# Kernel optimization log

Hardware: AMD Instinct MI355X
Metric: run time of the kernel (lower is better)

Reference implementation:

```python
import jax, jax.numpy as jnp
import numpy as np

NUM_FEATURES = 4
LATENT = 16
HIDDEN = 128
N_PIECES = 20
B, P = 8192, 128


def setup_inputs() -> dict:
    key = jax.random.key(0)
    ks = jax.random.split(key, 8)
    s = lambda fan_in: 1.0 / np.sqrt(fan_in)
    return {
        "x": jax.random.normal(ks[0], (B, P * NUM_FEATURES), jnp.float32),
        "W1": jax.random.normal(ks[1], (NUM_FEATURES, HIDDEN), jnp.float32) * s(NUM_FEATURES),
        "b1": jnp.zeros((HIDDEN,), jnp.float32),
        "W2": jax.random.normal(ks[2], (HIDDEN, HIDDEN), jnp.float32) * s(HIDDEN),
        "b2": jnp.zeros((HIDDEN,), jnp.float32),
        "W3": jax.random.normal(ks[3], (HIDDEN, 2 * LATENT), jnp.float32) * s(HIDDEN),
        "b3": jnp.zeros((2 * LATENT,), jnp.float32),
        "pool_weight": jax.random.normal(ks[4], (2 * LATENT, N_PIECES + 1), jnp.float32) * 0.1,
        "eps": jax.random.normal(ks[5], (B, LATENT), jnp.float32),
    }


def _fspool_weights(pool_weight, set_size):
    # piecewise-linear interpolation of pool_weight over normalized rank positions
    pos = jnp.arange(set_size, dtype=jnp.float32) / (set_size - 1) * N_PIECES  # [P]
    idx = jnp.clip(pos.astype(jnp.int32), 0, N_PIECES)
    frac = pos - idx.astype(jnp.float32)
    left = pool_weight[:, idx]                                   # [C, P]
    right = pool_weight[:, jnp.clip(idx + 1, 0, N_PIECES)]       # [C, P]
    return (1.0 - frac) * left + frac * right                    # [C, P]


def reference(x, W1, b1, W2, b2, W3, b3, pool_weight, eps):
    # per-particle shared MLP, batched over particles (B, P, F) -> (B, P, 2L)
    h = x.reshape(B, P, NUM_FEATURES)
    h = jax.nn.relu(jnp.einsum("bpf,fh->bph", h, W1) + b1)
    h = jax.nn.relu(jnp.einsum("bph,hk->bpk", h, W2) + b2)
    h = jnp.einsum("bph,hc->bpc", h, W3) + b3                    # [B, P, 2L]
    z = jnp.transpose(h, (0, 2, 1))                              # [B, 2L, P]
    # FSPool: descending featurewise sort + rank-weighted sum over set dim
    z_sorted = jnp.flip(jnp.sort(z, axis=-1), axis=-1)           # [B, 2L, P]
    w = _fspool_weights(pool_weight, P)                          # [2L, P]
    pooled = jnp.sum(z_sorted * w[None], axis=-1)                # [B, 2L]
    mus = pooled[:, ::2]
    logvars = pooled[:, 1::2]
    samples = mus + eps * jnp.exp(0.5 * logvars)
    return (mus, logvars, samples)
```

## Files before the change

kernel.cpp:

```cpp
#include <hip/hip_runtime.h>

#define B_TOT 8192
#define NB    16
#define NPCS  20

typedef __attribute__((ext_vector_type(8))) __fp16 f16x8;
typedef __attribute__((ext_vector_type(4))) float f32x4;
typedef __attribute__((ext_vector_type(2))) __fp16 fp16x2;

__device__ __forceinline__ unsigned pkmax(unsigned a, unsigned b) {
    unsigned d; asm("v_pk_max_f16 %0, %1, %2" : "=v"(d) : "v"(a), "v"(b)); return d;
}
__device__ __forceinline__ unsigned pkmin(unsigned a, unsigned b) {
    unsigned d; asm("v_pk_min_f16 %0, %1, %2" : "=v"(d) : "v"(a), "v"(b)); return d;
}
__device__ __forceinline__ unsigned pkrne(float a, float b) {
    fp16x2 h;
    h.x = (__fp16)a;
    h.y = (__fp16)b;
    return __builtin_bit_cast(unsigned, h);
}
__device__ __forceinline__ unsigned pkrtz(float a, float b) {
    return __builtin_bit_cast(unsigned, __builtin_amdgcn_cvt_pkrtz(a, b));
}
__device__ __forceinline__ float asf(unsigned u) { return __builtin_bit_cast(float, u); }
__device__ __forceinline__ unsigned asu(float f) { return __builtin_bit_cast(unsigned, f); }
__device__ __forceinline__ fp16x2 ash2(unsigned u) { return __builtin_bit_cast(fp16x2, u); }
__device__ __forceinline__ unsigned asu2(fp16x2 h) { return __builtin_bit_cast(unsigned, h); }

template<int CTRL>
__device__ __forceinline__ unsigned dppmov(unsigned v) {
    return (unsigned)__builtin_amdgcn_mov_dpp((int)v, CTRL, 0xf, 0xf, true);
}
__device__ __forceinline__ unsigned xlane(unsigned v, int lm) {
    switch (lm) {
    case 1:  return dppmov<0xB1>(v);
    case 2:  return dppmov<0x4E>(v);
    case 4:  return (unsigned)__builtin_amdgcn_ds_swizzle((int)v, 0x101F);
    default: return dppmov<0x128>(v);
    }
}
__device__ __forceinline__ float xlanef(float v, int lm) { return asf(xlane(asu(v), lm)); }

#define WS_W3T 32768
#define WS_WSP 40960
#define WS_W1A 57344
#define WS_B1F 61440

__device__ __forceinline__ unsigned packh2(float lo, float hi) {
    unsigned short a = __builtin_bit_cast(unsigned short, (__fp16)lo);
    unsigned short b = __builtin_bit_cast(unsigned short, (__fp16)hi);
    return (unsigned)a | ((unsigned)b << 16);
}

__device__ __forceinline__ int piperm(int j) {
    return (j & 0x60) | ((j & 0x0C) << 1) | ((j & 0x10) >> 2) | (j & 3);
}

__global__ void prep_kernel(const float* __restrict__ W1, const float* __restrict__ b1,
                            const float* __restrict__ W2, const float* __restrict__ W3,
                            const float* __restrict__ pw, void* __restrict__ ws)
{
    const int t = blockIdx.x * 256 + threadIdx.x;
    __fp16* w2t = (__fp16*)ws;
    __fp16* w3t = (__fp16*)((char*)ws + WS_W3T);
    float* wsp  = (float*)((char*)ws + WS_WSP);
    unsigned* w1a = (unsigned*)((char*)ws + WS_W1A);
    unsigned* b1f = (unsigned*)((char*)ws + WS_B1F);
    if (t < 16384) {
        int j = t >> 7, k = t & 127;
        w2t[t] = (__fp16)W2[k * 128 + piperm(j)];
    } else if (t < 20480) {
        int o = t - 16384, c = o >> 7, k = o & 127;
        w3t[o] = (__fp16)W3[k * 32 + c];
    } else if (t < 24576) {
        int o = t - 20480, c = o >> 7, p = o & 127;
        float pos = (float)p * (20.0f / 127.0f);
        int ip = min((int)pos, NPCS);
        float fr = pos - (float)ip;
        int ipb = min(ip + 1, NPCS);
        wsp[o] = (1.0f - fr) * pw[c * 21 + ip] + fr * pw[c * 21 + ipb];
    } else if (t < 25600) {
        int idx = t - 24576;
        int ht = idx >> 7, lane = (idx >> 1) & 63, pair = idx & 1;
        int quad = lane >> 4, l16 = lane & 15;
        unsigned val = 0;
        if (quad == 0) {
            int sh = piperm(16 * ht + l16);
            val = packh2(W1[(2 * pair) * 128 + sh], W1[(2 * pair + 1) * 128 + sh]);
        }
        w1a[idx] = val;
    } else if (t < 26112) {
        int idx = t - 25600;
        int ht = idx >> 6, lane = idx & 63;
        int quad = lane >> 4, l16 = lane & 15;
        unsigned val = 0;
        if (quad == 0) {
            int sh = piperm(16 * ht + l16);
            val = packh2(b1[sh], 0.0f);
        }
        b1f[idx] = val;
    }
}

#define L_SZP0 32768
#define L_SZP1 41216
#define L_POOL 49664

__global__ __launch_bounds__(256, 2) void enc_kernel(
    const float* __restrict__ x,   const float* __restrict__ b1g,
    const float* __restrict__ b2g, const float* __restrict__ b3g,
    const float* __restrict__ eps, const void* __restrict__ ws,
    float* __restrict__ out)
{
    __shared__ __align__(16) char smem[51712];

    const int tid  = threadIdx.x;
    const int wv   = tid >> 6;
    const int lane = tid & 63;
    const int l16  = lane & 15;
    const int quad = lane >> 4;
    const int b0   = blockIdx.x * NB;

    {
        const uint4* src = (const uint4*)ws;
#pragma unroll
        for (int it = 0; it < 8; ++it) {
            int idx = tid + it * 256;
            int j = idx >> 4, ch = idx & 15;
            *(uint4*)(smem + j * 256 + ((ch ^ (j & 15)) * 16)) = src[idx];
        }
    }

    f16x8 w3f[2][4];
    {
        const __fp16* w3t = (const __fp16*)((const char*)ws + WS_W3T);
#pragma unroll
        for (int mt2 = 0; mt2 < 2; ++mt2)
#pragma unroll
            for (int kt = 0; kt < 4; ++kt)
                w3f[mt2][kt] = *(const f16x8*)(w3t + (mt2 * 16 + l16) * 128 + kt * 32 + quad * 8);
    }
    union WF { unsigned u[4]; f16x8 v; } w1f[8];
    {
        const unsigned* w1a = (const unsigned*)((const char*)ws + WS_W1A);
        const unsigned* b1f = (const unsigned*)((const char*)ws + WS_B1F);
#pragma unroll
        for (int ht = 0; ht < 8; ++ht) {
            uint2 w01 = *(const uint2*)(w1a + ht * 128 + lane * 2);
            w1f[ht].u[0] = w01.x;
            w1f[ht].u[1] = w01.y;
            w1f[ht].u[2] = b1f[ht * 64 + lane];
            w1f[ht].u[3] = 0;
        }
    }
    f32x4 b3acc[2];
    {
        float4 t0 = *(const float4*)(b3g + quad * 4);
        float4 t1 = *(const float4*)(b3g + 16 + quad * 4);
        b3acc[0] = (f32x4){t0.x, t0.y, t0.z, t0.w};
        b3acc[1] = (f32x4){t1.x, t1.y, t1.z, t1.w};
    }
    f32x4 b2acc[8];
#pragma unroll
    for (int nt = 0; nt < 8; ++nt) {
        float4 t4 = *(const float4*)(b2g + (nt >> 1) * 32 + quad * 8 + (nt & 1) * 4);
        b2acc[nt] = (f32x4){t4.x, t4.y, t4.z, t4.w};
    }

    const int pr = wv * 4 + quad;
    float wE[8], wO[8];
    {
        const float* wsp = (const float*)((const char*)ws + WS_WSP);
        float4 e0 = *(const float4*)(wsp + (2 * pr) * 128 + l16 * 8);
        float4 e1 = *(const float4*)(wsp + (2 * pr) * 128 + l16 * 8 + 4);
        float4 o0 = *(const float4*)(wsp + (2 * pr + 1) * 128 + l16 * 8);
        float4 o1 = *(const float4*)(wsp + (2 * pr + 1) * 128 + l16 * 8 + 4);
        wE[0]=e0.x; wE[1]=e0.y; wE[2]=e0.z; wE[3]=e0.w; wE[4]=e1.x; wE[5]=e1.y; wE[6]=e1.z; wE[7]=e1.w;
        wO[0]=o0.x; wO[1]=o0.y; wO[2]=o0.z; wO[3]=o0.w; wO[4]=o1.x; wO[5]=o1.y; wO[6]=o1.z; wO[7]=o1.w;
    }

    const int ib = l16 * 8;
    const unsigned sfl8  = (ib & 8)  ? 0x80008000u : 0u;
    const unsigned sfl16 = (ib & 16) ? 0x80008000u : 0u;
    const unsigned sfl32 = (ib & 32) ? 0x80008000u : 0u;
    const unsigned sfl64 = (ib & 64) ? 0x80008000u : 0u;

    __syncthreads();

    unsigned* szpA  = (unsigned*)(smem + L_SZP0);
    unsigned* szpB  = (unsigned*)(smem + L_SZP1);
    float*    spool = (float*)(smem + L_POOL);

    union XB { unsigned u[4]; f16x8 v; } xb0, xb1;
    xb0.u[2] = 0x3C003C00u; xb0.u[3] = 0;
    xb1.u[2] = 0x3C003C00u; xb1.u[3] = 0;
    const f32x4 zc = (f32x4){0.f, 0.f, 0.f, 0.f};

    const float* xptr = x + (size_t)b0 * 512 + (wv * 32 + l16) * 4;
    float4 xv0 = *(const float4*)(xptr);
    float4 xv1 = *(const float4*)(xptr + 64);

    auto do_gemms = [&](unsigned* __restrict__ szpW, int pfIdx) {
        xb0.u[0] = pkrtz(xv0.x, xv0.y);
        xb0.u[1] = pkrtz(xv0.z, xv0.w);
        xb1.u[0] = pkrtz(xv1.x, xv1.y);
        xb1.u[1] = pkrtz(xv1.z, xv1.w);

        const int pfc = pfIdx < NB - 1 ? pfIdx : NB - 1;
        xv0 = *(const float4*)(xptr + pfc * 512);
        xv1 = *(const float4*)(xptr + pfc * 512 + 64);

        union AF { unsigned u[4]; f16x8 v; } a1[2][4];
#pragma unroll
        for (int ht = 0; ht < 8; ++ht) {
            f32x4 d0 = __builtin_amdgcn_mfma_f32_16x16x32_f16(w1f[ht].v, xb0.v, zc, 0, 0, 0);
            f32x4 d1 = __builtin_amdgcn_mfma_f32_16x16x32_f16(w1f[ht].v, xb1.v, zc, 0, 0, 0);
            const int kt = ht >> 1, jb = 2 * (ht & 1);
            a1[0][kt].u[jb]     = pkmax(pkrtz(d0[0], d0[1]), 0u);
            a1[0][kt].u[jb + 1] = pkmax(pkrtz(d0[2], d0[3]), 0u);
            a1[1][kt].u[jb]     = pkmax(pkrtz(d1[0], d1[1]), 0u);
            a1[1][kt].u[jb + 1] = pkmax(pkrtz(d1[2], d1[3]), 0u);
        }

        f32x4 acc2[2][8];
#pragma unroll
        for (int kt = 0; kt < 4; ++kt)
#pragma unroll
            for (int nt = 0; nt < 8; ++nt) {
                const int j = nt * 16 + l16;
                const int phys = (kt * 4 + quad) ^ l16;
                f16x8 wf = *(const f16x8*)(smem + j * 256 + phys * 16);
                if (kt == 0) {
                    acc2[0][nt] = __builtin_amdgcn_mfma_f32_16x16x32_f16(wf, a1[0][0].v, b2acc[nt], 0, 0, 0);
                    acc2[1][nt] = __builtin_amdgcn_mfma_f32_16x16x32_f16(wf, a1[1][0].v, b2acc[nt], 0, 0, 0);
                } else {
                    acc2[0][nt] = __builtin_amdgcn_mfma_f32_16x16x32_f16(wf, a1[0][kt].v, acc2[0][nt], 0, 0, 0);
                    acc2[1][nt] = __builtin_amdgcn_mfma_f32_16x16x32_f16(wf, a1[1][kt].v, acc2[1][nt], 0, 0, 0);
                }
            }

#pragma unroll
        for (int mt = 0; mt < 2; ++mt) {
            unsigned pkx[8], pky[8];
#pragma unroll
            for (int nt = 0; nt < 8; ++nt) {
                pkx[nt] = pkmax(pkrtz(acc2[mt][nt][0], acc2[mt][nt][1]), 0u);
                pky[nt] = pkmax(pkrtz(acc2[mt][nt][2], acc2[mt][nt][3]), 0u);
            }
            union A3 { unsigned u[4]; f16x8 v; } a3[4];
#pragma unroll
            for (int kt = 0; kt < 4; ++kt) {
                a3[kt].u[0] = pkx[2 * kt];
                a3[kt].u[1] = pky[2 * kt];
                a3[kt].u[2] = pkx[2 * kt + 1];
                a3[kt].u[3] = pky[2 * kt + 1];
            }
            const int colbase = wv * 32 + mt * 16;
#pragma unroll
            for (int mt2 = 0; mt2 < 2; ++mt2) {
                f32x4 acc = __builtin_amdgcn_mfma_f32_16x16x32_f16(w3f[mt2][0], a3[0].v, b3acc[mt2], 0, 0, 0);
#pragma unroll
                for (int kt = 1; kt < 4; ++kt)
                    acc = __builtin_amdgcn_mfma_f32_16x16x32_f16(w3f[mt2][kt], a3[kt].v, acc, 0, 0, 0);
                const int prw = 8 * mt2 + 2 * quad;
                szpW[prw * 132 + colbase + l16]       = pkrne(acc[0], acc[1]);
                szpW[(prw + 1) * 132 + colbase + l16] = pkrne(acc[2], acc[3]);
            }
        }
    };

    auto do_sort = [&](const unsigned* __restrict__ szpR, int e) {
        unsigned v[8];
        {
            const unsigned* zp = szpR + pr * 132 + l16 * 8;
            uint4 za = *(const uint4*)zp;
            uint4 zb = *(const uint4*)(zp + 4);
            v[0]=za.x; v[1]=za.y; v[2]=za.z; v[3]=za.w;
            v[4]=zb.x; v[5]=zb.y; v[6]=zb.z; v[7]=zb.w;
        }
#pragma unroll
        for (int k = 2; k <= 128; k <<= 1) {
#pragma unroll
            for (int j = 64; j >= 1; j >>= 1) {
                if (j >= k) continue;
                if (j >= 8) {
                    const bool km = ((ib & k) == 0) != ((ib & j) != 0);
                    const int lm = j >> 3;
#pragma unroll
                    for (int r = 0; r < 8; ++r) {
                        unsigned p = xlane(v[r], lm);
                        unsigned mx = pkmax(v[r], p), mn = pkmin(v[r], p);
                        v[r] = km ? mx : mn;
                    }
                } else if (k <= 4) {
#pragma unroll
                    for (int a = 0; a < 8; ++a) {
                        if (a & j) continue;
                        const int bx = a | j;
                        unsigned mx = pkmax(v[a], v[bx]), mn = pkmin(v[a], v[bx]);
                        if ((a & k) == 0) { v[a] = mx; v[bx] = mn; }
                        else              { v[a] = mn; v[bx] = mx; }
                    }
                } else {
                    const unsigned sfl = (k == 8) ? sfl8 : (k == 16) ? sfl16 :
                                         (k == 32) ? sfl32 : (k == 64) ? sfl64 : 0u;
                    if (j == 4 && k != 128) {
#pragma unroll
                        for (int r = 0; r < 8; ++r) v[r] ^= sfl;
                    }
#pragma unroll
                    for (int a = 0; a < 8; ++a) {
                        if (a & j) continue;
                        const int bx = a | j;
                        unsigned mx = pkmax(v[a], v[bx]), mn = pkmin(v[a], v[bx]);
                        v[a] = mx; v[bx] = mn;
                    }
                    if (j == 1 && k != 128) {
#pragma unroll
                        for (int r = 0; r < 8; ++r) v[r] ^= sfl;
                    }
                }
            }
        }

        float sE = 0.f, sO = 0.f;
#pragma unroll
        for (int r = 0; r < 8; ++r) {
            const fp16x2 hv = ash2(v[r]);
            sE = fmaf(wE[r], (float)hv.x, sE);
            sO = fmaf(wO[r], (float)hv.y, sO);
        }
#pragma unroll
        for (int d = 8; d >= 1; d >>= 1) {
            sE += xlanef(sE, d);
            sO += xlanef(sO, d);
        }
        if (l16 == 0) {
            spool[e * 32 + 2 * pr]     = sE;
            spool[e * 32 + 2 * pr + 1] = sO;
        }
    };

    do_gemms(szpA, 1);
    __syncthreads();

    for (int e = 0; e < NB - 1; ++e) {
        unsigned* srd = (e & 1) ? szpB : szpA;
        unsigned* dwr = (e & 1) ? szpA : szpB;
        do_gemms(dwr, e + 2);
        do_sort(srd, e);
        __syncthreads();
    }
    do_sort(((NB - 1) & 1) ? szpB : szpA, NB - 1);
    __syncthreads();

    {
        const int e = tid >> 4, t = tid & 15;
        const float mu = spool[e * 32 + 2 * t];
        const float lv = spool[e * 32 + 2 * t + 1];
        const float ev = eps[(size_t)b0 * 16 + tid];
        const float smp = fmaf(ev, __expf(0.5f * lv), mu);
        out[(size_t)b0 * 16 + tid] = mu;
        out[(size_t)B_TOT * 16 + (size_t)b0 * 16 + tid] = lv;
        out[(size_t)2 * B_TOT * 16 + (size_t)b0 * 16 + tid] = smp;
    }
}

extern "C" void kernel_launch(void* const* d_in, const int* in_sizes, int n_in,
                              void* d_out, int out_size, void* d_ws, size_t ws_size,
                              hipStream_t stream) {
    const float* x   = (const float*)d_in[0];
    const float* W1  = (const float*)d_in[1];
    const float* b1  = (const float*)d_in[2];
    const float* W2  = (const float*)d_in[3];
    const float* b2  = (const float*)d_in[4];
    const float* W3  = (const float*)d_in[5];
    const float* b3  = (const float*)d_in[6];
    const float* pw  = (const float*)d_in[7];
    const float* eps = (const float*)d_in[8];
    float* out = (float*)d_out;

    prep_kernel<<<dim3(102), dim3(256), 0, stream>>>(W1, b1, W2, W3, pw, d_ws);
    enc_kernel<<<dim3(B_TOT / NB), dim3(256), 0, stream>>>(x, b1, b2, b3, eps, d_ws, out);
}
```

Baseline: 145.7 us.

## Batch two events per sort phase and precompute W2 LDS addresses

The per-event software pipeline (GEMM for the next event overlapped with the sort of the current one, one barrier per event) is replaced by a phased loop. Each phase runs the GEMMs for two events into both buffers, synchronises, then sorts both events together with an interleaved bitonic network, then synchronises again. Sorting two independent sets at once exposes more instruction-level parallelism in the shuffle and min/max chains. The cost is losing the GEMM/sort overlap, doubling the barriers per event pair, and holding more live registers. W2 shared-memory addresses are also hoisted into precomputed per-kt pointers to cut index arithmetic in the inner loop.

```diff
diff --git a/kernel.cpp b/kernel.cpp
--- a/kernel.cpp
+++ b/kernel.cpp
@@ -192,6 +192,11 @@
     unsigned* szpB  = (unsigned*)(smem + L_SZP1);
     float*    spool = (float*)(smem + L_POOL);
 
+    const char* w2p[4];
+#pragma unroll
+    for (int kt = 0; kt < 4; ++kt)
+        w2p[kt] = smem + l16 * 256 + (((kt * 4 + quad) ^ l16) * 16);
+
     union XB { unsigned u[4]; f16x8 v; } xb0, xb1;
     xb0.u[2] = 0x3C003C00u; xb0.u[3] = 0;
     xb1.u[2] = 0x3C003C00u; xb1.u[3] = 0;
@@ -228,9 +233,7 @@
         for (int kt = 0; kt < 4; ++kt)
 #pragma unroll
             for (int nt = 0; nt < 8; ++nt) {
-                const int j = nt * 16 + l16;
-                const int phys = (kt * 4 + quad) ^ l16;
-                f16x8 wf = *(const f16x8*)(smem + j * 256 + phys * 16);
+                f16x8 wf = *(const f16x8*)(w2p[kt] + nt * 4096);
                 if (kt == 0) {
                     acc2[0][nt] = __builtin_amdgcn_mfma_f32_16x16x32_f16(wf, a1[0][0].v, b2acc[nt], 0, 0, 0);
                     acc2[1][nt] = __builtin_amdgcn_mfma_f32_16x16x32_f16(wf, a1[1][0].v, b2acc[nt], 0, 0, 0);
@@ -270,14 +273,19 @@
         }
     };
 
-    auto do_sort = [&](const unsigned* __restrict__ szpR, int e) {
-        unsigned v[8];
+    auto do_sort2 = [&](int e0) {
+        unsigned v[2][8];
         {
-            const unsigned* zp = szpR + pr * 132 + l16 * 8;
-            uint4 za = *(const uint4*)zp;
-            uint4 zb = *(const uint4*)(zp + 4);
-            v[0]=za.x; v[1]=za.y; v[2]=za.z; v[3]=za.w;
-            v[4]=zb.x; v[5]=zb.y; v[6]=zb.z; v[7]=zb.w;
+            const unsigned* zp0 = szpA + pr * 132 + l16 * 8;
+            uint4 za = *(const uint4*)zp0;
+            uint4 zb = *(const uint4*)(zp0 + 4);
+            v[0][0]=za.x; v[0][1]=za.y; v[0][2]=za.z; v[0][3]=za.w;
+            v[0][4]=zb.x; v[0][5]=zb.y; v[0][6]=zb.z; v[0][7]=zb.w;
+            const unsigned* zp1 = szpB + pr * 132 + l16 * 8;
+            uint4 zcd = *(const uint4*)zp1;
+            uint4 zd = *(const uint4*)(zp1 + 4);
+            v[1][0]=zcd.x; v[1][1]=zcd.y; v[1][2]=zcd.z; v[1][3]=zcd.w;
+            v[1][4]=zd.x;  v[1][5]=zd.y;  v[1][6]=zd.z;  v[1][7]=zd.w;
         }
 #pragma unroll
         for (int k = 2; k <= 128; k <<= 1) {
@@ -288,72 +296,84 @@
                     const bool km = ((ib & k) == 0) != ((ib & j) != 0);
                     const int lm = j >> 3;
 #pragma unroll
-                    for (int r = 0; r < 8; ++r) {
-                        unsigned p = xlane(v[r], lm);
-                        unsigned mx = pkmax(v[r], p), mn = pkmin(v[r], p);
-                        v[r] = km ? mx : mn;
-                    }
+                    for (int q = 0; q < 2; ++q)
+#pragma unroll
+                        for (int r = 0; r < 8; ++r) {
+                            unsigned p = xlane(v[q][r], lm);
+                            unsigned mx = pkmax(v[q][r], p), mn = pkmin(v[q][r], p);
+                            v[q][r] = km ? mx : mn;
+                        }
                 } else if (k <= 4) {
 #pragma unroll
-                    for (int a = 0; a < 8; ++a) {
-                        if (a & j) continue;
-                        const int bx = a | j;
-                        unsigned mx = pkmax(v[a], v[bx]), mn = pkmin(v[a], v[bx]);
-                        if ((a & k) == 0) { v[a] = mx; v[bx] = mn; }
-                        else              { v[a] = mn; v[bx] = mx; }
-                    }
+                    for (int q = 0; q < 2; ++q)
+#pragma unroll
+                        for (int a = 0; a < 8; ++a) {
+                            if (a & j) continue;
+                            const int bx = a | j;
+                            unsigned mx = pkmax(v[q][a], v[q][bx]), mn = pkmin(v[q][a], v[q][bx]);
+                            if ((a & k) == 0) { v[q][a] = mx; v[q][bx] = mn; }
+                            else              { v[q][a] = mn; v[q][bx] = mx; }
+                        }
                 } else {
                     const unsigned sfl = (k == 8) ? sfl8 : (k == 16) ? sfl16 :
                                          (k == 32) ? sfl32 : (k == 64) ? sfl64 : 0u;
                     if (j == 4 && k != 128) {
 #pragma unroll
-                        for (int r = 0; r < 8; ++r) v[r] ^= sfl;
+                        for (int q = 0; q < 2; ++q)
+#pragma unroll
+                            for (int r = 0; r < 8; ++r) v[q][r] ^= sfl;
                     }
 #pragma unroll
-                    for (int a = 0; a < 8; ++a) {
-                        if (a & j) continue;
-                        const int bx = a | j;
-                        unsigned mx = pkmax(v[a], v[bx]), mn = pkmin(v[a], v[bx]);
-                        v[a] = mx; v[bx] = mn;
-                    }
+                    for (int q = 0; q < 2; ++q)
+#pragma unroll
+                        for (int a = 0; a < 8; ++a) {
+                            if (a & j) continue;
+                            const int bx = a | j;
+                            unsigned mx = pkmax(v[q][a], v[q][bx]), mn = pkmin(v[q][a], v[q][bx]);
+                            v[q][a] = mx; v[q][bx] = mn;
+                        }
                     if (j == 1 && k != 128) {
 #pragma unroll
-                        for (int r = 0; r < 8; ++r) v[r] ^= sfl;
+                        for (int q = 0; q < 2; ++q)
+#pragma unroll
+                            for (int r = 0; r < 8; ++r) v[q][r] ^= sfl;
                     }
                 }
             }
         }
 
-        float sE = 0.f, sO = 0.f;
+        float sE0 = 0.f, sO0 = 0.f, sE1 = 0.f, sO1 = 0.f;
 #pragma unroll
         for (int r = 0; r < 8; ++r) {
-            const fp16x2 hv = ash2(v[r]);
-            sE = fmaf(wE[r], (float)hv.x, sE);
-            sO = fmaf(wO[r], (float)hv.y, sO);
+            const fp16x2 h0 = ash2(v[0][r]);
+            const fp16x2 h1 = ash2(v[1][r]);
+            sE0 = fmaf(wE[r], (float)h0.x, sE0);
+            sO0 = fmaf(wO[r], (float)h0.y, sO0);
+            sE1 = fmaf(wE[r], (float)h1.x, sE1);
+            sO1 = fmaf(wO[r], (float)h1.y, sO1);
         }
 #pragma unroll
         for (int d = 8; d >= 1; d >>= 1) {
-            sE += xlanef(sE, d);
-            sO += xlanef(sO, d);
+            sE0 += xlanef(sE0, d);
+            sO0 += xlanef(sO0, d);
+            sE1 += xlanef(sE1, d);
+            sO1 += xlanef(sO1, d);
         }
         if (l16 == 0) {
-            spool[e * 32 + 2 * pr]     = sE;
-            spool[e * 32 + 2 * pr + 1] = sO;
+            spool[e0 * 32 + 2 * pr]           = sE0;
+            spool[e0 * 32 + 2 * pr + 1]       = sO0;
+            spool[(e0 + 1) * 32 + 2 * pr]     = sE1;
+            spool[(e0 + 1) * 32 + 2 * pr + 1] = sO1;
         }
     };
 
-    do_gemms(szpA, 1);
-    __syncthreads();
-
-    for (int e = 0; e < NB - 1; ++e) {
-        unsigned* srd = (e & 1) ? szpB : szpA;
-        unsigned* dwr = (e & 1) ? szpA : szpB;
-        do_gemms(dwr, e + 2);
-        do_sort(srd, e);
+    for (int ep = 0; ep < NB; ep += 2) {
+        do_gemms(szpA, ep + 1);
+        do_gemms(szpB, ep + 2);
         __syncthreads();
-    }
-    do_sort(((NB - 1) & 1) ? szpB : szpA, NB - 1);
-    __syncthreads();
+        do_sort2(ep);
+        __syncthreads();
+    }
 
     {
         const int e = tid >> 4, t = tid & 15;
```

Result: no change. 146.9 us (+0.8%).

## Split fused encoder into separate MLP GEMM and sort-pool kernels via workspace

Applied to the files above, without the earlier changes.

Replaces the single fused MLP+FSPool kernel with two kernels when the workspace is large enough. The first runs the three-layer MLP with MFMA and writes packed fp16 latents to a global buffer. The second does a per-channel bitonic sort in registers using cross-lane swaps, then the weighted pooling and reparameterization. The aim is to let each stage use its own occupancy and tiling (8 batch items per GEMM block, 4 blocks/CU for sort) and avoid shared-memory staging between stages. The cost is an extra 64 MB global write and read, plus an extra launch.

```diff
diff --git a/kernel.cpp b/kernel.cpp
--- a/kernel.cpp
+++ b/kernel.cpp
@@ -2,6 +2,7 @@
 
 #define B_TOT 8192
 #define NB    16
+#define NBG   8
 #define NPCS  20
 
 typedef __attribute__((ext_vector_type(8))) __fp16 f16x8;
@@ -26,7 +27,6 @@
 __device__ __forceinline__ float asf(unsigned u) { return __builtin_bit_cast(float, u); }
 __device__ __forceinline__ unsigned asu(float f) { return __builtin_bit_cast(unsigned, f); }
 __device__ __forceinline__ fp16x2 ash2(unsigned u) { return __builtin_bit_cast(fp16x2, u); }
-__device__ __forceinline__ unsigned asu2(fp16x2 h) { return __builtin_bit_cast(unsigned, h); }
 
 template<int CTRL>
 __device__ __forceinline__ unsigned dppmov(unsigned v) {
@@ -46,6 +46,8 @@
 #define WS_WSP 40960
 #define WS_W1A 57344
 #define WS_B1F 61440
+#define WS_Z   65536
+#define Z_BYTES ((size_t)B_TOT * 16 * 128 * 4)
 
 __device__ __forceinline__ unsigned packh2(float lo, float hi) {
     unsigned short a = __builtin_bit_cast(unsigned short, (__fp16)lo);
@@ -103,11 +105,259 @@
     }
 }
 
+__global__ __launch_bounds__(256, 2) void enc_gemm_kernel(
+    const float* __restrict__ x, const float* __restrict__ b2g,
+    const float* __restrict__ b3g, void* __restrict__ ws)
+{
+    __shared__ __align__(16) char smem[32768];
+
+    const int tid  = threadIdx.x;
+    const int wv   = tid >> 6;
+    const int lane = tid & 63;
+    const int l16  = lane & 15;
+    const int quad = lane >> 4;
+    const int b0   = blockIdx.x * NBG;
+    unsigned* zg   = (unsigned*)((char*)ws + WS_Z);
+
+    {
+        const uint4* src = (const uint4*)ws;
+#pragma unroll
+        for (int it = 0; it < 8; ++it) {
+            int idx = tid + it * 256;
+            int j = idx >> 4, ch = idx & 15;
+            *(uint4*)(smem + j * 256 + ((ch ^ (j & 15)) * 16)) = src[idx];
+        }
+    }
+
+    f16x8 w3f[2][4];
+    {
+        const __fp16* w3t = (const __fp16*)((const char*)ws + WS_W3T);
+#pragma unroll
+        for (int mt2 = 0; mt2 < 2; ++mt2)
+#pragma unroll
+            for (int kt = 0; kt < 4; ++kt)
+                w3f[mt2][kt] = *(const f16x8*)(w3t + (mt2 * 16 + l16) * 128 + kt * 32 + quad * 8);
+    }
+    union WF { unsigned u[4]; f16x8 v; } w1f[8];
+    {
+        const unsigned* w1a = (const unsigned*)((const char*)ws + WS_W1A);
+        const unsigned* b1f = (const unsigned*)((const char*)ws + WS_B1F);
+#pragma unroll
+        for (int ht = 0; ht < 8; ++ht) {
+            uint2 w01 = *(const uint2*)(w1a + ht * 128 + lane * 2);
+            w1f[ht].u[0] = w01.x;
+            w1f[ht].u[1] = w01.y;
+            w1f[ht].u[2] = b1f[ht * 64 + lane];
+            w1f[ht].u[3] = 0;
+        }
+    }
+    f32x4 b3acc[2];
+    {
+        float4 t0 = *(const float4*)(b3g + quad * 4);
+        float4 t1 = *(const float4*)(b3g + 16 + quad * 4);
+        b3acc[0] = (f32x4){t0.x, t0.y, t0.z, t0.w};
+        b3acc[1] = (f32x4){t1.x, t1.y, t1.z, t1.w};
+    }
+    f32x4 b2acc[8];
+#pragma unroll
+    for (int nt = 0; nt < 8; ++nt) {
+        float4 t4 = *(const float4*)(b2g + (nt >> 1) * 32 + quad * 8 + (nt & 1) * 4);
+        b2acc[nt] = (f32x4){t4.x, t4.y, t4.z, t4.w};
+    }
+
+    __syncthreads();
+
+    const char* w2p[4];
+#pragma unroll
+    for (int kt = 0; kt < 4; ++kt)
+        w2p[kt] = smem + l16 * 256 + (((kt * 4 + quad) ^ l16) * 16);
+
+    union XB { unsigned u[4]; f16x8 v; } xb0, xb1;
+    xb0.u[2] = 0x3C003C00u; xb0.u[3] = 0;
+    xb1.u[2] = 0x3C003C00u; xb1.u[3] = 0;
+    const f32x4 zc = (f32x4){0.f, 0.f, 0.f, 0.f};
+
+    const float* xptr = x + (size_t)b0 * 512 + (wv * 32 + l16) * 4;
+    float4 xv0 = *(const float4*)(xptr);
+    float4 xv1 = *(const float4*)(xptr + 64);
+
+    for (int e = 0; e < NBG; ++e) {
+        xb0.u[0] = pkrtz(xv0.x, xv0.y);
+        xb0.u[1] = pkrtz(xv0.z, xv0.w);
+        xb1.u[0] = pkrtz(xv1.x, xv1.y);
+        xb1.u[1] = pkrtz(xv1.z, xv1.w);
+
+        const int pfc = e + 1 < NBG ? e + 1 : NBG - 1;
+        xv0 = *(const float4*)(xptr + pfc * 512);
+        xv1 = *(const float4*)(xptr + pfc * 512 + 64);
+
+        union AF { unsigned u[4]; f16x8 v; } a1[2][4];
+#pragma unroll
+        for (int ht = 0; ht < 8; ++ht) {
+            f32x4 d0 = __builtin_amdgcn_mfma_f32_16x16x32_f16(w1f[ht].v, xb0.v, zc, 0, 0, 0);
+            f32x4 d1 = __builtin_amdgcn_mfma_f32_16x16x32_f16(w1f[ht].v, xb1.v, zc, 0, 0, 0);
+            const int kt = ht >> 1, jb = 2 * (ht & 1);
+            a1[0][kt].u[jb]     = pkmax(pkrtz(d0[0], d0[1]), 0u);
+            a1[0][kt].u[jb + 1] = pkmax(pkrtz(d0[2], d0[3]), 0u);
+            a1[1][kt].u[jb]     = pkmax(pkrtz(d1[0], d1[1]), 0u);
+            a1[1][kt].u[jb + 1] = pkmax(pkrtz(d1[2], d1[3]), 0u);
+        }
+
+        f32x4 acc2[2][8];
+#pragma unroll
+        for (int kt = 0; kt < 4; ++kt)
+#pragma unroll
+            for (int nt = 0; nt < 8; ++nt) {
+                f16x8 wf = *(const f16x8*)(w2p[kt] + nt * 4096);
+                if (kt == 0) {
+                    acc2[0][nt] = __builtin_amdgcn_mfma_f32_16x16x32_f16(wf, a1[0][0].v, b2acc[nt], 0, 0, 0);
+                    acc2[1][nt] = __builtin_amdgcn_mfma_f32_16x16x32_f16(wf, a1[1][0].v, b2acc[nt], 0, 0, 0);
+                } else {
+                    acc2[0][nt] = __builtin_amdgcn_mfma_f32_16x16x32_f16(wf, a1[0][kt].v, acc2[0][nt], 0, 0, 0);
+                    acc2[1][nt] = __builtin_amdgcn_mfma_f32_16x16x32_f16(wf, a1[1][kt].v, acc2[1][nt], 0, 0, 0);
+                }
+            }
+
+        unsigned* zrow = zg + (size_t)(b0 + e) * (16 * 128);
+#pragma unroll
+        for (int mt = 0; mt < 2; ++mt) {
+            unsigned pkx[8], pky[8];
+#pragma unroll
+            for (int nt = 0; nt < 8; ++nt) {
+                pkx[nt] = pkmax(pkrtz(acc2[mt][nt][0], acc2[mt][nt][1]), 0u);
+                pky[nt] = pkmax(pkrtz(acc2[mt][nt][2], acc2[mt][nt][3]), 0u);
+            }
+            union A3 { unsigned u[4]; f16x8 v; } a3[4];
+#pragma unroll
+            for (int kt = 0; kt < 4; ++kt) {
+                a3[kt].u[0] = pkx[2 * kt];
+                a3[kt].u[1] = pky[2 * kt];
+                a3[kt].u[2] = pkx[2 * kt + 1];
+                a3[kt].u[3] = pky[2 * kt + 1];
+            }
+            const int colbase = wv * 32 + mt * 16;
+#pragma unroll
+            for (int mt2 = 0; mt2 < 2; ++mt2) {
+                f32x4 acc = __builtin_amdgcn_mfma_f32_16x16x32_f16(w3f[mt2][0], a3[0].v, b3acc[mt2], 0, 0, 0);
+#pragma unroll
+                for (int kt = 1; kt < 4; ++kt)
+                    acc = __builtin_amdgcn_mfma_f32_16x16x32_f16(w3f[mt2][kt], a3[kt].v, acc, 0, 0, 0);
+                const int prw = 8 * mt2 + 2 * quad;
+                zrow[prw * 128 + colbase + l16]       = pkrne(acc[0], acc[1]);
+                zrow[(prw + 1) * 128 + colbase + l16] = pkrne(acc[2], acc[3]);
+            }
+        }
+    }
+}
+
+__global__ __launch_bounds__(256, 4) void enc_sort_kernel(
+    const float* __restrict__ eps, const void* __restrict__ ws,
+    float* __restrict__ out)
+{
+    const int tid  = threadIdx.x;
+    const int wv   = tid >> 6;
+    const int lane = tid & 63;
+    const int l16  = lane & 15;
+    const int quad = lane >> 4;
+    const int t0   = blockIdx.x * 16 + wv * 4 + quad;
+    const int pr   = t0 & 15;
+    const unsigned* zg = (const unsigned*)((const char*)ws + WS_Z);
+
+    float wE[8], wO[8];
+    {
+        const float* wsp = (const float*)((const char*)ws + WS_WSP);
+        float4 e0 = *(const float4*)(wsp + (2 * pr) * 128 + l16 * 8);
+        float4 e1 = *(const float4*)(wsp + (2 * pr) * 128 + l16 * 8 + 4);
+        float4 o0 = *(const float4*)(wsp + (2 * pr + 1) * 128 + l16 * 8);
+        float4 o1 = *(const float4*)(wsp + (2 * pr + 1) * 128 + l16 * 8 + 4);
+        wE[0]=e0.x; wE[1]=e0.y; wE[2]=e0.z; wE[3]=e0.w; wE[4]=e1.x; wE[5]=e1.y; wE[6]=e1.z; wE[7]=e1.w;
+        wO[0]=o0.x; wO[1]=o0.y; wO[2]=o0.z; wO[3]=o0.w; wO[4]=o1.x; wO[5]=o1.y; wO[6]=o1.z; wO[7]=o1.w;
+    }
+
+    const int ib = l16 * 8;
+    const unsigned sfl8  = (ib & 8)  ? 0x80008000u : 0u;
+    const unsigned sfl16 = (ib & 16) ? 0x80008000u : 0u;
+    const unsigned sfl32 = (ib & 32) ? 0x80008000u : 0u;
+    const unsigned sfl64 = (ib & 64) ? 0x80008000u : 0u;
+
+    unsigned v[8];
+    {
+        const unsigned* zp = zg + (size_t)t0 * 128 + l16 * 8;
+        uint4 za = *(const uint4*)zp;
+        uint4 zb = *(const uint4*)(zp + 4);
+        v[0]=za.x; v[1]=za.y; v[2]=za.z; v[3]=za.w;
+        v[4]=zb.x; v[5]=zb.y; v[6]=zb.z; v[7]=zb.w;
+    }
+#pragma unroll
+    for (int k = 2; k <= 128; k <<= 1) {
+#pragma unroll
+        for (int j = 64; j >= 1; j >>= 1) {
+            if (j >= k) continue;
+            if (j >= 8) {
+                const bool km = ((ib & k) == 0) != ((ib & j) != 0);
+                const int lm = j >> 3;
+#pragma unroll
+                for (int r = 0; r < 8; ++r) {
+                    unsigned p = xlane(v[r], lm);
+                    unsigned mx = pkmax(v[r], p), mn = pkmin(v[r], p);
+                    v[r] = km ? mx : mn;
+                }
+            } else if (k <= 4) {
+#pragma unroll
+                for (int a = 0; a < 8; ++a) {
+                    if (a & j) continue;
+                    const int bx = a | j;
+                    unsigned mx = pkmax(v[a], v[bx]), mn = pkmin(v[a], v[bx]);
+                    if ((a & k) == 0) { v[a] = mx; v[bx] = mn; }
+                    else              { v[a] = mn; v[bx] = mx; }
+                }
+            } else {
+                const unsigned sfl = (k == 8) ? sfl8 : (k == 16) ? sfl16 :
+                                     (k == 32) ? sfl32 : (k == 64) ? sfl64 : 0u;
+                if (j == 4 && k != 128) {
+#pragma unroll
+                    for (int r = 0; r < 8; ++r) v[r] ^= sfl;
+                }
+#pragma unroll
+                for (int a = 0; a < 8; ++a) {
+                    if (a & j) continue;
+                    const int bx = a | j;
+                    unsigned mx = pkmax(v[a], v[bx]), mn = pkmin(v[a], v[bx]);
+                    v[a] = mx; v[bx] = mn;
+                }
+                if (j == 1 && k != 128) {
+#pragma unroll
+                    for (int r = 0; r < 8; ++r) v[r] ^= sfl;
+                }
+            }
+        }
+    }
+
+    float sE = 0.f, sO = 0.f;
+#pragma unroll
+    for (int r = 0; r < 8; ++r) {
+        const fp16x2 hv = ash2(v[r]);
+        sE = fmaf(wE[r], (float)hv.x, sE);
+        sO = fmaf(wO[r], (float)hv.y, sO);
+    }
+#pragma unroll
+    for (int d = 8; d >= 1; d >>= 1) {
+        sE += xlanef(sE, d);
+        sO += xlanef(sO, d);
+    }
+    if (l16 == 0) {
+        const float ev = eps[t0];
+        out[t0] = sE;
+        out[(size_t)B_TOT * 16 + t0] = sO;
+        out[(size_t)2 * B_TOT * 16 + t0] = fmaf(ev, __expf(0.5f * sO), sE);
+    }
+}
+
 #define L_SZP0 32768
 #define L_SZP1 41216
 #define L_POOL 49664
 
-__global__ __launch_bounds__(256, 2) void enc_kernel(
+__global__ __launch_bounds__(256, 2) void enc_fused_kernel(
     const float* __restrict__ x,   const float* __restrict__ b1g,
     const float* __restrict__ b2g, const float* __restrict__ b3g,
     const float* __restrict__ eps, const void* __restrict__ ws,
@@ -382,5 +632,11 @@
     float* out = (float*)d_out;
 
     prep_kernel<<<dim3(102), dim3(256), 0, stream>>>(W1, b1, W2, W3, pw, d_ws);
-    enc_kernel<<<dim3(B_TOT / NB), dim3(256), 0, stream>>>(x, b1, b2, b3, eps, d_ws, out);
-}
+
+    if (ws_size >= (size_t)WS_Z + Z_BYTES) {
+        enc_gemm_kernel<<<dim3(B_TOT / NBG), dim3(256), 0, stream>>>(x, b2, b3, d_ws);
+        enc_sort_kernel<<<dim3(B_TOT * 16 / 16), dim3(256), 0, stream>>>(eps, d_ws, out);
+    } else {
+        enc_fused_kernel<<<dim3(B_TOT / NB), dim3(256), 0, stream>>>(x, b1, b2, b3, eps, d_ws, out);
+    }
+}
```

After: 149.8 us. 1.03x slower.
